# Kernel optimization log

Measured on AMD Instinct MI355X. Metric: run time of the kernel, lower is better.

The kernel has to match this reference:

```python
import jax, jax.numpy as jnp
import numpy as np

D_MODEL = 128
N_HEADS = 8
D_K = D_MODEL // N_HEADS
N_NODES = 50000
N_EDGES = 800000


def setup_inputs() -> dict:
    key = jax.random.key(0)
    ks = jax.random.split(key, 8)
    X = jax.random.normal(ks[0], (N_NODES, D_MODEL), dtype=jnp.float32)
    nbr_src = jax.random.randint(ks[1], (N_EDGES,), 0, N_NODES, dtype=jnp.int32)
    nbr_dst = jax.random.randint(ks[2], (N_EDGES,), 0, N_NODES, dtype=jnp.int32)
    s = 1.0 / np.sqrt(D_MODEL)
    W_qkv = jax.random.normal(ks[3], (3 * D_MODEL, D_MODEL), dtype=jnp.float32) * s
    w_bias = jax.random.normal(ks[4], (N_HEADS, D_MODEL), dtype=jnp.float32) * s
    W_gate = jax.random.normal(ks[5], (D_MODEL, D_MODEL), dtype=jnp.float32) * s
    b_gate = jax.random.normal(ks[6], (D_MODEL,), dtype=jnp.float32) * s
    W_o = jax.random.normal(ks[7], (D_MODEL, D_MODEL), dtype=jnp.float32) * s
    return {"X": X, "W_qkv": W_qkv, "w_bias": w_bias, "W_gate": W_gate,
            "b_gate": b_gate, "W_o": W_o, "nbr_src": nbr_src,
            "nbr_dst": nbr_dst, "num_cells": N_NODES}


def segment_softmax(scores, seg, num_segments):
    # scores: [E, H], seg: [E] -> softmax over edges sharing the same seg id
    mx = jax.ops.segment_max(scores, seg, num_segments=num_segments)  # [N, H]
    mx = jnp.where(jnp.isfinite(mx), mx, -1e9)
    exp_s = jnp.exp(scores - mx[seg])
    sm = jax.ops.segment_sum(exp_s, seg, num_segments=num_segments)  # [N, H]
    return exp_s / (sm[seg] + 1e-12)


def reference(X, W_qkv, w_bias, W_gate, b_gate, W_o, nbr_src, nbr_dst, num_cells):
    H, dk = N_HEADS, D_K
    scale = 1.0 / np.sqrt(dk)
    qkv = (X @ W_qkv.T).reshape(-1, 3, H, dk)      # [N, 3, H, dk]
    Q, K, V = qkv[:, 0], qkv[:, 1], qkv[:, 2]
    gate = jax.nn.sigmoid(X @ W_gate.T + b_gate).reshape(-1, H, dk)
    bias = X @ w_bias.T                             # [N, H]
    scores = jnp.einsum('ehd,ehd->eh', Q[nbr_src], K[nbr_dst]) * scale + bias[nbr_src]
    attn = segment_softmax(scores, nbr_src, num_cells)          # [E, H]
    out = jax.ops.segment_sum(attn[:, :, None] * V[nbr_dst], nbr_src,
                              num_segments=num_cells)           # [N, H, dk]
    return (gate * out).reshape(-1, D_MODEL) @ W_o.T
```

## Files before the change

kernel.cpp:

```cpp
#include <hip/hip_runtime.h>
#include <hip/hip_fp16.h>

#define DM 128
#define NHEADS 8
#define MAXDEG 64
#define SROW 136

typedef _Float16 half8 __attribute__((ext_vector_type(8)));
typedef _Float16 half2v __attribute__((ext_vector_type(2)));
typedef float floatx4 __attribute__((ext_vector_type(4)));

union H8 { half8 v; half2v h2[4]; };

__global__ __launch_bounds__(256) void proj_csr(
    const float* __restrict__ X, const float* __restrict__ Wqkv,
    const float* __restrict__ Wgate, const float* __restrict__ wbias,
    const float* __restrict__ b_gate,
    const int* __restrict__ nsrc, const int* __restrict__ ndst,
    int* __restrict__ cnt, int* __restrict__ csr_dst,
    _Float16* __restrict__ Q, _Float16* __restrict__ KV,
    _Float16* __restrict__ gate, float* __restrict__ bias,
    int M, int E, int P) {
  __shared__ _Float16 As[128 * SROW];
  __shared__ _Float16 Bs[64 * SROW];
  int tid = threadIdx.x;
  int bid = blockIdx.x;

  if (bid >= P) {
    int ebase = (bid - P) * 8192;
    for (int g = 0; g < 4; g++) {
      int s[8], d[8];
#pragma unroll
      for (int j = 0; j < 8; j++) {
        int e = ebase + (g * 8 + j) * 256 + tid;
        s[j] = (e < E) ? nsrc[e] : -1;
        d[j] = (e < E) ? ndst[e] : 0;
      }
#pragma unroll
      for (int j = 0; j < 8; j++) {
        if (s[j] >= 0) {
          int p = atomicAdd(&cnt[s[j]], 1);
          if (p < MAXDEG) csr_dst[(size_t)s[j] * MAXDEG + p] = d[j];
        }
      }
    }
    return;
  }

  int m0 = bid * 128;

#pragma unroll
  for (int i = 0; i < 4; i++) {
    int u = tid + i * 256;
    int r = u >> 3;
    int cc = (u & 7) * 16;
    int gr = m0 + r;
    float4 f0, f1, f2, f3;
    if (gr < M) {
      const float4* src = (const float4*)(X + (size_t)gr * 128 + cc);
      f0 = src[0]; f1 = src[1]; f2 = src[2]; f3 = src[3];
    } else {
      f0 = f1 = f2 = f3 = make_float4(0.f, 0.f, 0.f, 0.f);
    }
    half8 h0 = {(_Float16)f0.x, (_Float16)f0.y, (_Float16)f0.z, (_Float16)f0.w,
                (_Float16)f1.x, (_Float16)f1.y, (_Float16)f1.z, (_Float16)f1.w};
    half8 h1 = {(_Float16)f2.x, (_Float16)f2.y, (_Float16)f2.z, (_Float16)f2.w,
                (_Float16)f3.x, (_Float16)f3.y, (_Float16)f3.z, (_Float16)f3.w};
    *(half8*)(As + r * SROW + cc) = h0;
    *(half8*)(As + r * SROW + cc + 8) = h1;
  }

  int wid = tid >> 6, lane = tid & 63;
  int quad = lane >> 4, l16 = lane & 15;
  int mw = wid * 32;

  for (int c = 0; c < 9; c++) {
    __syncthreads();
#pragma unroll
    for (int i = 0; i < 4; i++) {
      int u = tid + i * 256;
      int r = u >> 4;
      int cc = (u & 15) * 8;
      int grow = c * 64 + r;
      const float* src = nullptr;
      if (grow < 384)      src = Wqkv + (size_t)grow * 128 + cc;
      else if (grow < 512) src = Wgate + (size_t)(grow - 384) * 128 + cc;
      else if (grow < 520) src = wbias + (size_t)(grow - 512) * 128 + cc;
      half8 h = {};
      if (src) {
        float4 f0 = ((const float4*)src)[0];
        float4 f1 = ((const float4*)src)[1];
        h = half8{(_Float16)f0.x, (_Float16)f0.y, (_Float16)f0.z, (_Float16)f0.w,
                  (_Float16)f1.x, (_Float16)f1.y, (_Float16)f1.z, (_Float16)f1.w};
      }
      *(half8*)(Bs + r * SROW + cc) = h;
    }
    __syncthreads();

    floatx4 acc[2][4] = {};
#pragma unroll
    for (int kc = 0; kc < 4; kc++) {
      int ko = kc * 32 + quad * 8;
      half8 a0 = *(const half8*)(As + (mw + l16) * SROW + ko);
      half8 a1 = *(const half8*)(As + (mw + 16 + l16) * SROW + ko);
      half8 b[4];
#pragma unroll
      for (int ni = 0; ni < 4; ni++)
        b[ni] = *(const half8*)(Bs + (ni * 16 + l16) * SROW + ko);
#pragma unroll
      for (int ni = 0; ni < 4; ni++) {
        acc[0][ni] = __builtin_amdgcn_mfma_f32_16x16x32_f16(a0, b[ni], acc[0][ni], 0, 0, 0);
        acc[1][ni] = __builtin_amdgcn_mfma_f32_16x16x32_f16(a1, b[ni], acc[1][ni], 0, 0, 0);
      }
    }

    if (c == 8) {
      if (l16 < 8) {
#pragma unroll
        for (int mi = 0; mi < 2; mi++)
#pragma unroll
          for (int r = 0; r < 4; r++) {
            int row = m0 + mw + mi * 16 + quad * 4 + r;
            if (row < M) bias[(size_t)row * 8 + l16] = acc[mi][0][r];
          }
      }
    } else {
      int reg = c >> 1;
#pragma unroll
      for (int mi = 0; mi < 2; mi++) {
#pragma unroll
        for (int ni = 0; ni < 4; ni++) {
          int colL = (c & 1) * 64 + ni * 16 + l16;
#pragma unroll
          for (int r = 0; r < 4; r++) {
            int row = m0 + mw + mi * 16 + quad * 4 + r;
            if (row >= M) continue;
            float v = acc[mi][ni][r];
            if (reg == 0)      Q[(size_t)row * 128 + colL] = (_Float16)v;
            else if (reg == 1) KV[(size_t)row * 256 + colL] = (_Float16)v;
            else if (reg == 2) KV[(size_t)row * 256 + 128 + colL] = (_Float16)v;
            else gate[(size_t)row * 128 + colL] =
                   (_Float16)(1.0f / (1.0f + __expf(-(v + b_gate[colL]))));
          }
        }
      }
    }
  }
}

__global__ __launch_bounds__(256) void final_gemm_mfma(
    const _Float16* __restrict__ A, const float* __restrict__ Wo,
    float* __restrict__ C, int M) {
  __shared__ _Float16 As[128 * SROW];
  __shared__ _Float16 Bs[64 * SROW];
  int tid = threadIdx.x;
  int m0 = blockIdx.x * 128, n0 = blockIdx.y * 64;
#pragma unroll
  for (int i = 0; i < 8; i++) {
    int u = tid + i * 256;
    int r = u >> 4;
    int cc = (u & 15) * 8;
    int gr = m0 + r;
    int4 val = make_int4(0, 0, 0, 0);
    if (gr < M) val = *(const int4*)(A + (size_t)gr * 128 + cc);
    *(int4*)(As + r * SROW + cc) = val;
  }
#pragma unroll
  for (int i = 0; i < 4; i++) {
    int u = tid + i * 256;
    int r = u >> 4;
    int cc = (u & 15) * 8;
    const float* src = Wo + (size_t)(n0 + r) * 128 + cc;
    float4 f0 = ((const float4*)src)[0];
    float4 f1 = ((const float4*)src)[1];
    half8 h = {(_Float16)f0.x, (_Float16)f0.y, (_Float16)f0.z, (_Float16)f0.w,
               (_Float16)f1.x, (_Float16)f1.y, (_Float16)f1.z, (_Float16)f1.w};
    *(half8*)(Bs + r * SROW + cc) = h;
  }
  __syncthreads();

  int wid = tid >> 6, lane = tid & 63;
  int quad = lane >> 4, l16 = lane & 15;
  int mw = (wid >> 1) * 64;
  int nw = (wid & 1) * 32;

  floatx4 acc[4][2] = {};
#pragma unroll
  for (int kc = 0; kc < 4; kc++) {
    int ko = kc * 32 + quad * 8;
    half8 a[4], b[2];
#pragma unroll
    for (int mi = 0; mi < 4; mi++)
      a[mi] = *(const half8*)(As + (mw + mi * 16 + l16) * SROW + ko);
#pragma unroll
    for (int ni = 0; ni < 2; ni++)
      b[ni] = *(const half8*)(Bs + (nw + ni * 16 + l16) * SROW + ko);
#pragma unroll
    for (int mi = 0; mi < 4; mi++)
#pragma unroll
      for (int ni = 0; ni < 2; ni++)
        acc[mi][ni] = __builtin_amdgcn_mfma_f32_16x16x32_f16(a[mi], b[ni], acc[mi][ni], 0, 0, 0);
  }
#pragma unroll
  for (int mi = 0; mi < 4; mi++) {
#pragma unroll
    for (int ni = 0; ni < 2; ni++) {
      int col = n0 + nw + ni * 16 + l16;
#pragma unroll
      for (int r = 0; r < 4; r++) {
        int row = m0 + mw + mi * 16 + quad * 4 + r;
        if (row >= M) continue;
        C[(size_t)row * 128 + col] = acc[mi][ni][r];
      }
    }
  }
}

__global__ __launch_bounds__(256) void attn_fused(
    const int* __restrict__ cnt, const int* __restrict__ csr_dst,
    const _Float16* __restrict__ Q, const _Float16* __restrict__ KV,
    const float* __restrict__ bias, const _Float16* __restrict__ gate,
    _Float16* __restrict__ gated, int N) {
  int wave = threadIdx.x >> 6, lane = threadIdx.x & 63;
  int n = blockIdx.x * 4 + wave;
  if (n >= N) return;
  int deg = cnt[n];
  if (deg > MAXDEG) deg = MAXDEG;
  int qtr = lane >> 4, l16 = lane & 15;
  int ch0 = l16 * 8;

  int dstv = csr_dst[(size_t)n * MAXDEG + lane];

  H8 qu; qu.v = *(const half8*)(Q + (size_t)n * DM + ch0);
  float bias_h = bias[(size_t)n * NHEADS + (l16 >> 1)];

  float acc[8] = {};
  float den = 0.f;
  int iters = (deg + 3) >> 2;

  H8 k0, v0, k1, v1;
  k0.v = half8{}; v0.v = half8{}; k1.v = half8{}; v1.v = half8{};
  bool b0 = false, b1 = false;
  if (0 < iters) {
    int e = qtr;
    b0 = e < deg;
    int d = __shfl(dstv, e);
    d = b0 ? d : 0;
    const _Float16* kvp = KV + (size_t)d * 256 + ch0;
    k0.v = *(const half8*)kvp;
    v0.v = *(const half8*)(kvp + 128);
  }
  if (1 < iters) {
    int e = 4 + qtr;
    b1 = e < deg;
    int d = __shfl(dstv, e);
    d = b1 ? d : 0;
    const _Float16* kvp = KV + (size_t)d * 256 + ch0;
    k1.v = *(const half8*)kvp;
    v1.v = *(const half8*)(kvp + 128);
  }

  for (int it = 0; it < iters; it++) {
    H8 k2, v2;
    k2.v = half8{}; v2.v = half8{};
    bool b2 = false;
    if (it + 2 < iters) {
      int e = (it + 2) * 4 + qtr;
      b2 = e < deg;
      int d = __shfl(dstv, e);
      d = b2 ? d : 0;
      const _Float16* kvp = KV + (size_t)d * 256 + ch0;
      k2.v = *(const half8*)kvp;
      v2.v = *(const half8*)(kvp + 128);
    }
    float p = 0.f;
#pragma unroll
    for (int j = 0; j < 4; j++)
      p = __builtin_amdgcn_fdot2(qu.h2[j], k0.h2[j], p, false);
    p += __shfl_xor(p, 1);
    float w = __expf(p * 0.25f + bias_h);
    if (!b0) w = 0.f;
    den += w;
#pragma unroll
    for (int j = 0; j < 8; j++) acc[j] = fmaf(w, (float)v0.v[j], acc[j]);
    k0 = k1; v0 = v1; b0 = b1;
    k1 = k2; v1 = v2; b1 = b2;
  }
#pragma unroll
  for (int j = 0; j < 8; j++) acc[j] += __shfl_xor(acc[j], 16);
#pragma unroll
  for (int j = 0; j < 8; j++) acc[j] += __shfl_xor(acc[j], 32);
  den += __shfl_xor(den, 16);
  den += __shfl_xor(den, 32);

  if (qtr == 0) {
    float inv = 1.0f / (den + 1e-12f);
    half8 gv = *(const half8*)(gate + (size_t)n * DM + ch0);
    half8 o;
#pragma unroll
    for (int j = 0; j < 8; j++) o[j] = (_Float16)(acc[j] * inv * (float)gv[j]);
    *(half8*)(gated + (size_t)n * DM + ch0) = o;
  }
}

extern "C" void kernel_launch(void* const* d_in, const int* in_sizes, int n_in,
                              void* d_out, int out_size, void* d_ws, size_t ws_size,
                              hipStream_t stream) {
  const float* X     = (const float*)d_in[0];
  const float* Wqkv  = (const float*)d_in[1];
  const float* wbias = (const float*)d_in[2];
  const float* Wgate = (const float*)d_in[3];
  const float* bgate = (const float*)d_in[4];
  const float* Wo    = (const float*)d_in[5];
  const int*   nsrc  = (const int*)d_in[6];
  const int*   ndst  = (const int*)d_in[7];
  int N = in_sizes[0] / 128;
  int E = in_sizes[6];
  float* out = (float*)d_out;

  char* p = (char*)d_ws;
  _Float16* Q16     = (_Float16*)p; p += (size_t)N * 128 * sizeof(_Float16);
  _Float16* KV16    = (_Float16*)p; p += (size_t)N * 256 * sizeof(_Float16);
  _Float16* gate16  = (_Float16*)p; p += (size_t)N * 128 * sizeof(_Float16);
  _Float16* gated16 = (_Float16*)p; p += (size_t)N * 128 * sizeof(_Float16);
  float* bias       = (float*)p;    p += (size_t)N * 8 * sizeof(float);
  int* cnt          = (int*)p;      p += (size_t)N * sizeof(int);
  int* csr_dst      = (int*)p;      p += (size_t)N * MAXDEG * sizeof(int);

  hipMemsetAsync(cnt, 0, (size_t)N * sizeof(int), stream);

  int P = (N + 127) / 128;
  int C = (E + 8191) / 8192;
  proj_csr<<<P + C, 256, 0, stream>>>(X, Wqkv, Wgate, wbias, bgate, nsrc, ndst,
                                      cnt, csr_dst, Q16, KV16, gate16, bias, N, E, P);

  attn_fused<<<(N + 3) / 4, 256, 0, stream>>>(cnt, csr_dst, Q16, KV16, bias,
                                              gate16, gated16, N);

  dim3 fg((N + 127) / 128, 2);
  final_gemm_mfma<<<fg, 256, 0, stream>>>(gated16, Wo, out, N);
}
```

Baseline: 217.4 us.

## Pad degree counters to separate cache lines and simplify attention prefetch

Measured after the change: 229.1 us. 1.05x slower.

```diff
diff --git a/kernel.cpp b/kernel.cpp
--- a/kernel.cpp
+++ b/kernel.cpp
@@ -4,13 +4,18 @@
 #define DM 128
 #define NHEADS 8
 #define MAXDEG 64
+#define CNTSTRIDE 16
 #define SROW 136
 
 typedef _Float16 half8 __attribute__((ext_vector_type(8)));
-typedef _Float16 half2v __attribute__((ext_vector_type(2)));
 typedef float floatx4 __attribute__((ext_vector_type(4)));
 
-union H8 { half8 v; half2v h2[4]; };
+union H8 { half8 v; _Float16 h[8]; };
+
+__device__ inline half8 cvt8(const float4 f0, const float4 f1) {
+  return half8{(_Float16)f0.x, (_Float16)f0.y, (_Float16)f0.z, (_Float16)f0.w,
+               (_Float16)f1.x, (_Float16)f1.y, (_Float16)f1.z, (_Float16)f1.w};
+}
 
 __global__ __launch_bounds__(256) void proj_csr(
     const float* __restrict__ X, const float* __restrict__ Wqkv,
@@ -39,7 +44,7 @@
 #pragma unroll
       for (int j = 0; j < 8; j++) {
         if (s[j] >= 0) {
-          int p = atomicAdd(&cnt[s[j]], 1);
+          int p = atomicAdd(&cnt[(size_t)s[j] * CNTSTRIDE], 1);
           if (p < MAXDEG) csr_dst[(size_t)s[j] * MAXDEG + p] = d[j];
         }
       }
@@ -62,12 +67,8 @@
     } else {
       f0 = f1 = f2 = f3 = make_float4(0.f, 0.f, 0.f, 0.f);
     }
-    half8 h0 = {(_Float16)f0.x, (_Float16)f0.y, (_Float16)f0.z, (_Float16)f0.w,
-                (_Float16)f1.x, (_Float16)f1.y, (_Float16)f1.z, (_Float16)f1.w};
-    half8 h1 = {(_Float16)f2.x, (_Float16)f2.y, (_Float16)f2.z, (_Float16)f2.w,
-                (_Float16)f3.x, (_Float16)f3.y, (_Float16)f3.z, (_Float16)f3.w};
-    *(half8*)(As + r * SROW + cc) = h0;
-    *(half8*)(As + r * SROW + cc + 8) = h1;
+    *(half8*)(As + r * SROW + cc) = cvt8(f0, f1);
+    *(half8*)(As + r * SROW + cc + 8) = cvt8(f2, f3);
   }
 
   int wid = tid >> 6, lane = tid & 63;
@@ -87,12 +88,7 @@
       else if (grow < 512) src = Wgate + (size_t)(grow - 384) * 128 + cc;
       else if (grow < 520) src = wbias + (size_t)(grow - 512) * 128 + cc;
       half8 h = {};
-      if (src) {
-        float4 f0 = ((const float4*)src)[0];
-        float4 f1 = ((const float4*)src)[1];
-        h = half8{(_Float16)f0.x, (_Float16)f0.y, (_Float16)f0.z, (_Float16)f0.w,
-                  (_Float16)f1.x, (_Float16)f1.y, (_Float16)f1.z, (_Float16)f1.w};
-      }
+      if (src) h = cvt8(((const float4*)src)[0], ((const float4*)src)[1]);
       *(half8*)(Bs + r * SROW + cc) = h;
     }
     __syncthreads();
@@ -148,6 +144,82 @@
   }
 }
 
+__global__ __launch_bounds__(256) void attn_fused(
+    const int* __restrict__ cnt, const int* __restrict__ csr_dst,
+    const _Float16* __restrict__ Q, const _Float16* __restrict__ KV,
+    const float* __restrict__ bias, const _Float16* __restrict__ gate,
+    _Float16* __restrict__ gated, int N) {
+  int wave = threadIdx.x >> 6, lane = threadIdx.x & 63;
+  int n = blockIdx.x * 4 + wave;
+  if (n >= N) return;
+  int deg = cnt[(size_t)n * CNTSTRIDE];
+  if (deg > MAXDEG) deg = MAXDEG;
+  int qtr = lane >> 4, l16 = lane & 15;
+  int ch0 = l16 * 8;
+
+  int dstv = csr_dst[(size_t)n * MAXDEG + lane];
+
+  H8 qu; qu.v = *(const half8*)(Q + (size_t)n * DM + ch0);
+  float qf[8];
+#pragma unroll
+  for (int j = 0; j < 8; j++) qf[j] = (float)qu.h[j];
+  float bias_h = bias[(size_t)n * NHEADS + (l16 >> 1)];
+
+  float acc[8] = {};
+  float den = 0.f;
+  int iters = (deg + 3) >> 2;
+
+  H8 kc, vc; kc.v = half8{}; vc.v = half8{};
+  bool bc = false;
+  if (iters > 0) {
+    bc = qtr < deg;
+    int d = __shfl(dstv, qtr);
+    d = bc ? d : 0;
+    const _Float16* kvp = KV + (size_t)d * 256 + ch0;
+    kc.v = *(const half8*)kvp;
+    vc.v = *(const half8*)(kvp + 128);
+  }
+  for (int it = 0; it < iters; it++) {
+    H8 kn, vn; kn.v = half8{}; vn.v = half8{};
+    bool bn = false;
+    if (it + 1 < iters) {
+      int e = (it + 1) * 4 + qtr;
+      bn = e < deg;
+      int d = __shfl(dstv, e);
+      d = bn ? d : 0;
+      const _Float16* kvp = KV + (size_t)d * 256 + ch0;
+      kn.v = *(const half8*)kvp;
+      vn.v = *(const half8*)(kvp + 128);
+    }
+    float p = 0.f;
+#pragma unroll
+    for (int j = 0; j < 8; j++) p += qf[j] * (float)kc.h[j];
+    p += __shfl_xor(p, 1);
+    float w = __expf(p * 0.25f + bias_h);
+    if (!bc) w = 0.f;
+    den += w;
+#pragma unroll
+    for (int j = 0; j < 8; j++) acc[j] = fmaf(w, (float)vc.h[j], acc[j]);
+    kc = kn; vc = vn; bc = bn;
+  }
+#pragma unroll
+  for (int j = 0; j < 8; j++) {
+    acc[j] += __shfl_xor(acc[j], 16);
+    acc[j] += __shfl_xor(acc[j], 32);
+  }
+  den += __shfl_xor(den, 16);
+  den += __shfl_xor(den, 32);
+
+  if (qtr == 0) {
+    float inv = 1.0f / (den + 1e-12f);
+    H8 gv; gv.v = *(const half8*)(gate + (size_t)n * DM + ch0);
+    half8 o;
+#pragma unroll
+    for (int j = 0; j < 8; j++) o[j] = (_Float16)(acc[j] * inv * (float)gv.h[j]);
+    *(half8*)(gated + (size_t)n * DM + ch0) = o;
+  }
+}
+
 __global__ __launch_bounds__(256) void final_gemm_mfma(
     const _Float16* __restrict__ A, const float* __restrict__ Wo,
     float* __restrict__ C, int M) {
@@ -171,11 +243,7 @@
     int r = u >> 4;
     int cc = (u & 15) * 8;
     const float* src = Wo + (size_t)(n0 + r) * 128 + cc;
-    float4 f0 = ((const float4*)src)[0];
-    float4 f1 = ((const float4*)src)[1];
-    half8 h = {(_Float16)f0.x, (_Float16)f0.y, (_Float16)f0.z, (_Float16)f0.w,
-               (_Float16)f1.x, (_Float16)f1.y, (_Float16)f1.z, (_Float16)f1.w};
-    *(half8*)(Bs + r * SROW + cc) = h;
+    *(half8*)(Bs + r * SROW + cc) = cvt8(((const float4*)src)[0], ((const float4*)src)[1]);
   }
   __syncthreads();
 
@@ -213,93 +281,6 @@
         C[(size_t)row * 128 + col] = acc[mi][ni][r];
       }
     }
-  }
-}
-
-__global__ __launch_bounds__(256) void attn_fused(
-    const int* __restrict__ cnt, const int* __restrict__ csr_dst,
-    const _Float16* __restrict__ Q, const _Float16* __restrict__ KV,
-    const float* __restrict__ bias, const _Float16* __restrict__ gate,
-    _Float16* __restrict__ gated, int N) {
-  int wave = threadIdx.x >> 6, lane = threadIdx.x & 63;
-  int n = blockIdx.x * 4 + wave;
-  if (n >= N) return;
-  int deg = cnt[n];
-  if (deg > MAXDEG) deg = MAXDEG;
-  int qtr = lane >> 4, l16 = lane & 15;
-  int ch0 = l16 * 8;
-
-  int dstv = csr_dst[(size_t)n * MAXDEG + lane];
-
-  H8 qu; qu.v = *(const half8*)(Q + (size_t)n * DM + ch0);
-  float bias_h = bias[(size_t)n * NHEADS + (l16 >> 1)];
-
-  float acc[8] = {};
-  float den = 0.f;
-  int iters = (deg + 3) >> 2;
-
-  H8 k0, v0, k1, v1;
-  k0.v = half8{}; v0.v = half8{}; k1.v = half8{}; v1.v = half8{};
-  bool b0 = false, b1 = false;
-  if (0 < iters) {
-    int e = qtr;
-    b0 = e < deg;
-    int d = __shfl(dstv, e);
-    d = b0 ? d : 0;
-    const _Float16* kvp = KV + (size_t)d * 256 + ch0;
-    k0.v = *(const half8*)kvp;
-    v0.v = *(const half8*)(kvp + 128);
-  }
-  if (1 < iters) {
-    int e = 4 + qtr;
-    b1 = e < deg;
-    int d = __shfl(dstv, e);
-    d = b1 ? d : 0;
-    const _Float16* kvp = KV + (size_t)d * 256 + ch0;
-    k1.v = *(const half8*)kvp;
-    v1.v = *(const half8*)(kvp + 128);
-  }
-
-  for (int it = 0; it < iters; it++) {
-    H8 k2, v2;
-    k2.v = half8{}; v2.v = half8{};
-    bool b2 = false;
-    if (it + 2 < iters) {
-      int e = (it + 2) * 4 + qtr;
-      b2 = e < deg;
-      int d = __shfl(dstv, e);
-      d = b2 ? d : 0;
-      const _Float16* kvp = KV + (size_t)d * 256 + ch0;
-      k2.v = *(const half8*)kvp;
-      v2.v = *(const half8*)(kvp + 128);
-    }
-    float p = 0.f;
-#pragma unroll
-    for (int j = 0; j < 4; j++)
-      p = __builtin_amdgcn_fdot2(qu.h2[j], k0.h2[j], p, false);
-    p += __shfl_xor(p, 1);
-    float w = __expf(p * 0.25f + bias_h);
-    if (!b0) w = 0.f;
-    den += w;
-#pragma unroll
-    for (int j = 0; j < 8; j++) acc[j] = fmaf(w, (float)v0.v[j], acc[j]);
-    k0 = k1; v0 = v1; b0 = b1;
-    k1 = k2; v1 = v2; b1 = b2;
-  }
-#pragma unroll
-  for (int j = 0; j < 8; j++) acc[j] += __shfl_xor(acc[j], 16);
-#pragma unroll
-  for (int j = 0; j < 8; j++) acc[j] += __shfl_xor(acc[j], 32);
-  den += __shfl_xor(den, 16);
-  den += __shfl_xor(den, 32);
-
-  if (qtr == 0) {
-    float inv = 1.0f / (den + 1e-12f);
-    half8 gv = *(const half8*)(gate + (size_t)n * DM + ch0);
-    half8 o;
-#pragma unroll
-    for (int j = 0; j < 8; j++) o[j] = (_Float16)(acc[j] * inv * (float)gv[j]);
-    *(half8*)(gated + (size_t)n * DM + ch0) = o;
   }
 }
 
@@ -324,10 +305,10 @@
   _Float16* gate16  = (_Float16*)p; p += (size_t)N * 128 * sizeof(_Float16);
   _Float16* gated16 = (_Float16*)p; p += (size_t)N * 128 * sizeof(_Float16);
   float* bias       = (float*)p;    p += (size_t)N * 8 * sizeof(float);
-  int* cnt          = (int*)p;      p += (size_t)N * sizeof(int);
+  int* cnt          = (int*)p;      p += (size_t)N * CNTSTRIDE * sizeof(int);
   int* csr_dst      = (int*)p;      p += (size_t)N * MAXDEG * sizeof(int);
 
-  hipMemsetAsync(cnt, 0, (size_t)N * sizeof(int), stream);
+  hipMemsetAsync(cnt, 0, (size_t)N * CNTSTRIDE * sizeof(int), stream);
 
   int P = (N + 127) / 128;
   int C = (E + 8191) / 8192;
```
